# Performance work log

Hardware: AMD Instinct MI355X
Metric: run time of the kernel (lower is better)

Reference implementation:

```python
import jax, jax.numpy as jnp
import numpy as np

B, L, IN, D, H = 128, 64, 2, 256, 512  # batch, max_len, input_size, dense_size, hidden_size
A_S2S, A_PTR = H, D  # attention hidden sizes (defaults: hidden_size / dense_size)


def setup_inputs() -> dict:
    key = jax.random.key(0)
    ks = jax.random.split(key, 24)
    s = 0.05
    inp = {
        'inputs': jax.random.normal(ks[0], (B, L, IN), jnp.float32),
        'lengths': jax.random.randint(ks[1], (B,), L // 2, L + 1),
        'targets': jax.random.randint(ks[2], (B, L), 0, L),
        # input_dense: input_size -> dense_size
        'W_in': jax.random.normal(ks[3], (D, IN)) * s,
        'b_in': jnp.zeros((D,)),
        # encoder GRU (input D, hidden H), PyTorch layout [3H, in]
        'enc_Wi': jax.random.normal(ks[4], (3 * H, D)) * s,
        'enc_Wh': jax.random.normal(ks[5], (3 * H, H)) * s,
        'enc_bi': jnp.zeros((3 * H,)),
        'enc_bh': jnp.zeros((3 * H,)),
        # decoder GRU (input D+H, hidden H)
        'dec_Wi': jax.random.normal(ks[6], (3 * H, D + H)) * s,
        'dec_Wh': jax.random.normal(ks[7], (3 * H, H)) * s,
        'dec_bi': jnp.zeros((3 * H,)),
        'dec_bh': jnp.zeros((3 * H,)),
        # Bahdanau seq2seq attention: query_hidden = rnn_layers*H
        's2s_Wq': jax.random.normal(ks[8], (H, A_S2S)) * s,
        's2s_Wk': jax.random.normal(ks[9], (H, A_S2S)) * s,
        's2s_v': jax.random.normal(ks[10], (A_S2S,)) * s,
        # output_dense: hidden -> dense
        'W_out': jax.random.normal(ks[11], (D, H)) * s,
        'b_out': jnp.zeros((D,)),
        # Bahdanau pointer attention over dense_inputs
        'ptr_Wq': jax.random.normal(ks[12], (D, A_PTR)) * s,
        'ptr_Wk': jax.random.normal(ks[13], (D, A_PTR)) * s,
        'ptr_v': jax.random.normal(ks[14], (A_PTR,)) * s,
    }
    return inp


def _gru_cell(x, h, Wi, Wh, bi, bh):
    gi = x @ Wi.T + bi
    gh = h @ Wh.T + bh
    i_r, i_z, i_n = jnp.split(gi, 3, axis=-1)
    h_r, h_z, h_n = jnp.split(gh, 3, axis=-1)
    r = jax.nn.sigmoid(i_r + h_r)
    z = jax.nn.sigmoid(i_z + h_z)
    n = jnp.tanh(i_n + r * h_n)
    return (1.0 - z) * n + z * h


NEG = -1e9


def reference(inputs, lengths, targets, W_in, b_in, enc_Wi, enc_Wh, enc_bi, enc_bh,
              dec_Wi, dec_Wh, dec_bi, dec_bh, s2s_Wq, s2s_Wk, s2s_v,
              W_out, b_out, ptr_Wq, ptr_Wk, ptr_v):
    # teacher_forcing_prob fixed at 1.0 for determinism (uses targets each step)
    dense_inputs = inputs @ W_in.T + b_in            # [B, L, D]
    padding_mask = jnp.arange(L)[None, :] < lengths[:, None]  # [B, L] bool

    # ---- encoder (dynamic_rnn): run GRU over time, take hidden at lengths-1 ----
    def enc_step(h, x_t):
        h2 = _gru_cell(x_t, h, enc_Wi, enc_Wh, enc_bi, enc_bh)
        return h2, h2
    _, hs = jax.lax.scan(enc_step, jnp.zeros((B, H), dense_inputs.dtype),
                         dense_inputs.transpose(1, 0, 2))  # hs: [L, B, H]
    enc_out = hs.transpose(1, 0, 2) * padding_mask[:, :, None]  # zero padded steps
    hidden0 = hs[lengths - 1, jnp.arange(B)]  # final valid hidden, [B, H]

    # Precompute attention key projections (loop-invariant)
    enc_keys = enc_out @ s2s_Wk        # [B, L, A_S2S]
    ptr_keys = dense_inputs @ ptr_Wk   # [B, L, A_PTR]

    def dec_step(carry, inp):
        h, idx, step_mask = carry              # h [B,H], idx [B] int, step_mask [B,L]
        pm_i, tgt_i = inp                      # [B] bool, [B] int
        dec_in = dense_inputs[jnp.arange(B), idx]  # [B, D] gather
        m = pm_i[:, None] & padding_mask           # [B, L]
        # Bahdanau seq2seq attention, query = current hidden state
        q = h @ s2s_Wq                              # [B, A]
        scores = jnp.tanh(q[:, None, :] + enc_keys) @ s2s_v   # [B, L]
        scores = jnp.where(m, scores, NEG)
        w = jax.nn.softmax(scores, axis=-1)
        context = jnp.einsum('bl,blh->bh', w, enc_out)         # [B, H]
        x = jnp.concatenate([context, dec_in], axis=-1)        # [B, H+D]
        h_new = _gru_cell(x, h, dec_Wi, dec_Wh, dec_bi, dec_bh)
        # pointer attention over dense_inputs
        dense_out = h_new @ W_out.T + b_out                    # [B, D]
        p_mask = (step_mask > 0) & m
        pq = dense_out @ ptr_Wq
        plogit = jnp.tanh(pq[:, None, :] + ptr_keys) @ ptr_v   # [B, L]
        plogit = jnp.where(p_mask, plogit, NEG)
        pred = jnp.argmax(plogit, axis=-1)
        next_idx = tgt_i  # teacher forcing
        step_mask_new = step_mask * (1 - jax.nn.one_hot(next_idx, L, dtype=step_mask.dtype))
        return (h_new, next_idx, step_mask_new), (plogit, pred)

    carry0 = (hidden0, jnp.zeros((B,), jnp.int32),
              jnp.ones((B, L), jnp.int32))
    xs = (padding_mask.T, targets.T.astype(jnp.int32))
    _, (logits_t, preds_t) = jax.lax.scan(dec_step, carry0, xs)
    logits = logits_t.transpose(1, 0, 2)       # [B, L, L]
    predictions = preds_t.T                    # [B, L]
    return logits, predictions
```

## Files before the change

### kernel.cpp

```cpp
#include <hip/hip_runtime.h>

#define BB 128
#define LL 64
#define DD 256
#define HH 512
#define NEGC (-1e9f)

#define OFF_DENSE   0
#define OFF_ENCOUT  2097152
#define OFF_ENCKEYS 6291456
#define OFF_PTRKEYS 10485760
#define OFF_X       12582912
#define OFF_HB0     12681216
#define OFF_HB1     12746752
#define OFF_H0      12812288
#define OFF_Q       12877824
#define OFF_PQ      12943360
#define OFF_WQT     12976128
#define OFF_MT      13238272
#define OFF_BQ      13369344
#define OFF_SMASK   13369600

__device__ __forceinline__ float fast_tanh(float x) {
  float e = __expf(2.0f * x);
  return 1.0f - 2.0f / (e + 1.0f);
}
__device__ __forceinline__ float sigmoidf_(float x) {
  return 1.0f / (1.0f + __expf(-x));
}
__device__ __forceinline__ float wsum(float v) {
#pragma unroll
  for (int o = 32; o > 0; o >>= 1) v += __shfl_xor(v, o);
  return v;
}

#define D4(acc) fmaf(xv.x, w.x, fmaf(xv.y, w.y, fmaf(xv.z, w.z, fmaf(xv.w, w.w, acc))))


__global__ __launch_bounds__(256)
void k_init(const float* __restrict__ inp, const float* __restrict__ W_in,
            const float* __restrict__ b_in, float* __restrict__ dense,
            float* __restrict__ hb0, int* __restrict__ smask) {
  int idx = blockIdx.x * 256 + threadIdx.x;
  if (idx < BB * LL * DD) {
    int bl = idx >> 8, d = idx & 255;
    dense[idx] = fmaf(inp[bl * 2], W_in[d * 2], fmaf(inp[bl * 2 + 1], W_in[d * 2 + 1], b_in[d]));
  } else if (idx < BB * LL * DD + BB * HH) {
    hb0[idx - BB * LL * DD] = 0.f;
  } else if (idx < BB * LL * DD + BB * HH + BB * LL) {
    smask[idx - BB * LL * DD - BB * HH] = 1;
  }
}

__global__ __launch_bounds__(256)
void k_tr(const float* __restrict__ Wq, float* __restrict__ Wqt) {
  int idx = blockIdx.x * 256 + threadIdx.x;
  int h = idx >> 9, a = idx & 511;
  Wqt[a * 512 + h] = Wq[idx];
}

__global__ __launch_bounds__(512)
void k_mt(const float* __restrict__ W_out, const float* __restrict__ ptr_Wq,
          const float* __restrict__ b_out, float* __restrict__ Mt, float* __restrict__ bqv) {
  int a = blockIdx.x, tid = threadIdx.x;
  if (a < 256) {
    float acc = 0.f;
    for (int d = 0; d < 256; ++d) acc = fmaf(W_out[d * 512 + tid], ptr_Wq[d * 256 + a], acc);
    Mt[a * 512 + tid] = acc;
  } else if (tid < 256) {
    float acc = 0.f;
    for (int d = 0; d < 256; ++d) acc = fmaf(b_out[d], ptr_Wq[d * 256 + tid], acc);
    bqv[tid] = acc;
  }
}

__global__ __launch_bounds__(256)
void k_ptrkeys(const float* __restrict__ dense, const float* __restrict__ Wk,
               float* __restrict__ keys) {
  __shared__ float s[16 * 256];
  int r0 = blockIdx.x * 16, tid = threadIdx.x;
  for (int idx = tid; idx < 16 * 256; idx += 256) s[idx] = dense[r0 * 256 + idx];
  __syncthreads();
  float acc[16];
#pragma unroll
  for (int ri = 0; ri < 16; ++ri) acc[ri] = 0.f;
  for (int d = 0; d < 256; ++d) {
    float w = Wk[d * 256 + tid];
#pragma unroll
    for (int ri = 0; ri < 16; ++ri) acc[ri] = fmaf(s[ri * 256 + d], w, acc[ri]);
  }
#pragma unroll
  for (int ri = 0; ri < 16; ++ri) keys[(r0 + ri) * 256 + tid] = acc[ri];
}

__global__ __launch_bounds__(512)
void k_enckeys(const float* __restrict__ enc_out, const float* __restrict__ Wk,
               float* __restrict__ keys) {
  __shared__ float s[16 * 512];
  int r0 = blockIdx.x * 16, tid = threadIdx.x;
  for (int idx = tid; idx < 16 * 512; idx += 512) s[idx] = enc_out[r0 * 512 + idx];
  __syncthreads();
  float acc[16];
#pragma unroll
  for (int ri = 0; ri < 16; ++ri) acc[ri] = 0.f;
  for (int h = 0; h < 512; ++h) {
    float w = Wk[h * 512 + tid];
#pragma unroll
    for (int ri = 0; ri < 16; ++ri) acc[ri] = fmaf(s[ri * 512 + h], w, acc[ri]);
  }
#pragma unroll
  for (int ri = 0; ri < 16; ++ri) keys[(r0 + ri) * 512 + tid] = acc[ri];
}

__global__ __launch_bounds__(256)
void k_copy(const float* __restrict__ src, float* __restrict__ dst) {
  int idx = blockIdx.x * 256 + threadIdx.x;
  if (idx < BB * HH) dst[idx] = src[idx];
}

__global__ __launch_bounds__(256)
void k_enc(const float* __restrict__ dense, const float* __restrict__ hin,
           float* __restrict__ hout, const float* __restrict__ Wi,
           const float* __restrict__ Wh, const float* __restrict__ bi,
           const float* __restrict__ bh, const int* __restrict__ lengths,
           float* __restrict__ enc_out, float* __restrict__ h0, int t) {
  __shared__ float xs[16 * 772];
  __shared__ float part[2 * 16 * 8 * 8];
  const int tid = threadIdx.x;
  const int b0 = blockIdx.x * 16, u0 = blockIdx.y * 16;
  for (int idx = tid; idx < 16 * 768; idx += 256) {
    int bl = idx / 768, k = idx - bl * 768;
    xs[bl * 772 + k] = (k < 512) ? hin[(b0 + bl) * 512 + k]
                                 : dense[((b0 + bl) * 64 + t) * 256 + (k - 512)];
  }
  __syncthreads();
  {
    const int b_l = tid & 15, og = (tid >> 4) & 7, kp = tid >> 7;
    const int ua = u0 + og * 2;
    float ar0 = 0, az0 = 0, ain0 = 0, ahn0 = 0, ar1 = 0, az1 = 0, ain1 = 0, ahn1 = 0;
    const float* xr = xs + b_l * 772;
    const int k0 = kp * 384, k1 = k0 + 384;
    const int kA = (k1 < 512) ? k1 : 512;
    for (int k = k0; k < kA; k += 4) {
      float4 xv = *(const float4*)(xr + k);
      float4 w;
      w = *(const float4*)(Wh + (ua) * 512 + k);        ar0  = D4(ar0);
      w = *(const float4*)(Wh + (512 + ua) * 512 + k);  az0  = D4(az0);
      w = *(const float4*)(Wh + (1024 + ua) * 512 + k); ahn0 = D4(ahn0);
      w = *(const float4*)(Wh + (ua + 1) * 512 + k);    ar1  = D4(ar1);
      w = *(const float4*)(Wh + (513 + ua) * 512 + k);  az1  = D4(az1);
      w = *(const float4*)(Wh + (1025 + ua) * 512 + k); ahn1 = D4(ahn1);
    }
    const int kB = (k0 > 512) ? k0 : 512;
    for (int k = kB; k < k1; k += 4) {
      float4 xv = *(const float4*)(xr + k);
      float4 w;
      w = *(const float4*)(Wi + (ua) * 256 + k - 512);        ar0  = D4(ar0);
      w = *(const float4*)(Wi + (512 + ua) * 256 + k - 512);  az0  = D4(az0);
      w = *(const float4*)(Wi + (1024 + ua) * 256 + k - 512); ain0 = D4(ain0);
      w = *(const float4*)(Wi + (ua + 1) * 256 + k - 512);    ar1  = D4(ar1);
      w = *(const float4*)(Wi + (513 + ua) * 256 + k - 512);  az1  = D4(az1);
      w = *(const float4*)(Wi + (1025 + ua) * 256 + k - 512); ain1 = D4(ain1);
    }
    float* pp = part + ((kp * 16 + b_l) * 8 + og) * 8;
    pp[0] = ar0; pp[1] = az0; pp[2] = ain0; pp[3] = ahn0;
    pp[4] = ar1; pp[5] = az1; pp[6] = ain1; pp[7] = ahn1;
  }
  __syncthreads();
  {
    const int b_l = tid & 15, u_l = tid >> 4;
    const int og = u_l >> 1, uu = u_l & 1;
    const float* p0 = part + ((0 * 16 + b_l) * 8 + og) * 8 + uu * 4;
    const float* p1 = part + ((1 * 16 + b_l) * 8 + og) * 8 + uu * 4;
    float ar = p0[0] + p1[0], az = p0[1] + p1[1];
    float ain = p0[2] + p1[2], ahn = p0[3] + p1[3];
    const int u = u0 + u_l, b = b0 + b_l;
    float r = sigmoidf_(ar + bi[u] + bh[u]);
    float z = sigmoidf_(az + bi[512 + u] + bh[512 + u]);
    float n = fast_tanh(ain + bi[1024 + u] + r * (ahn + bh[1024 + u]));
    float hp = xs[b_l * 772 + u];
    float hn = (1.f - z) * n + z * hp;
    hout[b * 512 + u] = hn;
    int lenb = lengths[b];
    enc_out[(b * 64 + t) * 512 + u] = (t < lenb) ? hn : 0.f;
    if (t == lenb - 1) h0[b * 512 + u] = hn;
  }
}

__global__ __launch_bounds__(256)
void k_p1(int step, const float* __restrict__ qbuf, const float* __restrict__ pqbuf,
          const float* __restrict__ enc_keys, const float* __restrict__ ptr_keys,
          const float* __restrict__ enc_out, const float* __restrict__ dense,
          const float* __restrict__ s2s_v, const float* __restrict__ ptr_v,
          const int* __restrict__ lengths, const int* __restrict__ targets,
          int* __restrict__ smask, float* __restrict__ xbuf,
          float* __restrict__ logits, float* __restrict__ preds) {
  __shared__ float sq[512], sv[512], sl[64], wl[64];
  const int b = blockIdx.x, tid = threadIdx.x;
  const int wv = tid >> 6, ln = tid & 63;
  const int lenb = lengths[b];
  if (step > 0) {
    const int j = step - 1;
    sq[tid] = pqbuf[b * 256 + (tid & 255)];
    sv[tid] = ptr_v[tid & 255];
    __syncthreads();
#pragma unroll 4
    for (int li = 0; li < 16; ++li) {
      int l = wv * 16 + li;
      float acc = 0.f;
#pragma unroll
      for (int c = 0; c < 4; ++c) {
        int a = c * 64 + ln;
        acc = fmaf(fast_tanh(sq[a] + ptr_keys[(b * 64 + l) * 256 + a]), sv[a], acc);
      }
      acc = wsum(acc);
      if (ln == 0) sl[l] = acc;
    }
    __syncthreads();
    if (tid < 64) {
      int l = tid;
      bool pm = (j < lenb) && (l < lenb) && (smask[b * 64 + l] != 0);
      float v = pm ? sl[l] : NEGC;
      logits[(b * 64 + j) * 64 + l] = v;
      float bv = v; int bidx = l;
#pragma unroll
      for (int off = 32; off > 0; off >>= 1) {
        float ov = __shfl_xor(bv, off);
        int oi = __shfl_xor(bidx, off);
        if (ov > bv || (ov == bv && oi < bidx)) { bv = ov; bidx = oi; }
      }
      if (l == 0) preds[b * 64 + j] = (float)bidx;
    }
    __syncthreads();
    if (tid == 0) smask[b * 64 + targets[b * 64 + j]] = 0;
    __syncthreads();
  }
  if (step < 64) {
    const int i = step;
    sq[tid] = qbuf[b * 512 + tid];
    sq[tid + 256] = qbuf[b * 512 + 256 + tid];
    sv[tid] = s2s_v[tid];
    sv[tid + 256] = s2s_v[256 + tid];
    __syncthreads();
#pragma unroll 2
    for (int li = 0; li < 16; ++li) {
      int l = wv * 16 + li;
      float acc = 0.f;
#pragma unroll
      for (int c = 0; c < 8; ++c) {
        int a = c * 64 + ln;
        acc = fmaf(fast_tanh(sq[a] + enc_keys[(b * 64 + l) * 512 + a]), sv[a], acc);
      }
      acc = wsum(acc);
      if (ln == 0) sl[l] = ((i < lenb) && (l < lenb)) ? acc : NEGC;
    }
    __syncthreads();
    if (tid < 64) {
      float v = sl[tid];
      float m = v;
#pragma unroll
      for (int off = 32; off > 0; off >>= 1) m = fmaxf(m, __shfl_xor(m, off));
      float e = __expf(v - m);
      float s = e;
#pragma unroll
      for (int off = 32; off > 0; off >>= 1) s += __shfl_xor(s, off);
      wl[tid] = e / s;
    }
    __syncthreads();
    for (int hh = tid; hh < 512; hh += 256) {
      float c = 0.f;
#pragma unroll 8
      for (int l = 0; l < 64; ++l) c = fmaf(wl[l], enc_out[(b * 64 + l) * 512 + hh], c);
      xbuf[b * 768 + hh] = c;
    }
    int idx = (i == 0) ? 0 : targets[b * 64 + i - 1];
    xbuf[b * 768 + 512 + tid] = dense[(b * 64 + idx) * 256 + tid];
  }
}

__global__ __launch_bounds__(256)
void k_p2(const float* __restrict__ xbuf, const float* __restrict__ hin,
          float* __restrict__ hout, const float* __restrict__ Wi,
          const float* __restrict__ Wh, const float* __restrict__ bi,
          const float* __restrict__ bh) {
  __shared__ float xs[8 * 1284];
  __shared__ float part[4 * 8 * 8 * 8];
  const int tid = threadIdx.x;
  const int b0 = blockIdx.x * 8, u0 = blockIdx.y * 16;
  for (int idx = tid; idx < 8 * 1280; idx += 256) {
    int bl = idx / 1280, k = idx - bl * 1280;
    xs[bl * 1284 + k] = (k < 768) ? xbuf[(b0 + bl) * 768 + k]
                                  : hin[(b0 + bl) * 512 + (k - 768)];
  }
  __syncthreads();
  {
    const int b_l = tid & 7, og = (tid >> 3) & 7, kp = tid >> 6;
    const int ua = u0 + og * 2;
    float ar0 = 0, az0 = 0, ain0 = 0, ahn0 = 0, ar1 = 0, az1 = 0, ain1 = 0, ahn1 = 0;
    const float* xr = xs + b_l * 1284;
    const int k0 = kp * 320, k1 = k0 + 320;
    const int kA = (k1 < 768) ? k1 : 768;
    for (int k = k0; k < kA; k += 4) {
      float4 xv = *(const float4*)(xr + k);
      float4 w;
      w = *(const float4*)(Wi + (ua) * 768 + k);        ar0  = D4(ar0);
      w = *(const float4*)(Wi + (512 + ua) * 768 + k);  az0  = D4(az0);
      w = *(const float4*)(Wi + (1024 + ua) * 768 + k); ain0 = D4(ain0);
      w = *(const float4*)(Wi + (ua + 1) * 768 + k);    ar1  = D4(ar1);
      w = *(const float4*)(Wi + (513 + ua) * 768 + k);  az1  = D4(az1);
      w = *(const float4*)(Wi + (1025 + ua) * 768 + k); ain1 = D4(ain1);
    }
    const int kB = (k0 > 768) ? k0 : 768;
    for (int k = kB; k < k1; k += 4) {
      float4 xv = *(const float4*)(xr + k);
      float4 w;
      w = *(const float4*)(Wh + (ua) * 512 + k - 768);        ar0  = D4(ar0);
      w = *(const float4*)(Wh + (512 + ua) * 512 + k - 768);  az0  = D4(az0);
      w = *(const float4*)(Wh + (1024 + ua) * 512 + k - 768); ahn0 = D4(ahn0);
      w = *(const float4*)(Wh + (ua + 1) * 512 + k - 768);    ar1  = D4(ar1);
      w = *(const float4*)(Wh + (513 + ua) * 512 + k - 768);  az1  = D4(az1);
      w = *(const float4*)(Wh + (1025 + ua) * 512 + k - 768); ahn1 = D4(ahn1);
    }
    float* pp = part + ((kp * 8 + b_l) * 8 + og) * 8;
    pp[0] = ar0; pp[1] = az0; pp[2] = ain0; pp[3] = ahn0;
    pp[4] = ar1; pp[5] = az1; pp[6] = ain1; pp[7] = ahn1;
  }
  __syncthreads();
  if (tid < 128) {
    const int b_l = tid & 7, u_l = tid >> 3;
    const int og = u_l >> 1, uu = u_l & 1;
    float ar = 0, az = 0, ain = 0, ahn = 0;
#pragma unroll
    for (int kp = 0; kp < 4; ++kp) {
      const float* p = part + ((kp * 8 + b_l) * 8 + og) * 8 + uu * 4;
      ar += p[0]; az += p[1]; ain += p[2]; ahn += p[3];
    }
    const int u = u0 + u_l, b = b0 + b_l;
    float r = sigmoidf_(ar + bi[u] + bh[u]);
    float z = sigmoidf_(az + bi[512 + u] + bh[512 + u]);
    float n = fast_tanh(ain + bi[1024 + u] + r * (ahn + bh[1024 + u]));
    float hp = xs[b_l * 1284 + 768 + u];
    hout[b * 512 + u] = (1.f - z) * n + z * hp;
  }
}

__global__ __launch_bounds__(256)
void k_p3(const float* __restrict__ hsrc, const float* __restrict__ Wqt,
          const float* __restrict__ Mt, const float* __restrict__ bqv,
          float* __restrict__ qbuf, float* __restrict__ pqbuf) {
  __shared__ float hs[16 * 516];
  __shared__ float part[8 * 16 * 8];
  const int tid = threadIdx.x;
  const int b0 = blockIdx.x * 16, o0 = blockIdx.y * 8;
  for (int idx = tid; idx < 16 * 512; idx += 256) {
    int bl = idx >> 9, k = idx & 511;
    hs[bl * 516 + k] = hsrc[(b0 + bl) * 512 + k];
  }
  __syncthreads();
  {
    const int b_l = tid & 15, og = (tid >> 4) & 1, kp = tid >> 5;
    const int ob = o0 + og * 4;
    const float* w0 = (ob < 512) ? (Wqt + (ob) * 512) : (Mt + (ob - 512) * 512);
    const float* w1 = (ob < 512) ? (Wqt + (ob + 1) * 512) : (Mt + (ob - 511) * 512);
    const float* w2 = (ob < 512) ? (Wqt + (ob + 2) * 512) : (Mt + (ob - 510) * 512);
    const float* w3 = (ob < 512) ? (Wqt + (ob + 3) * 512) : (Mt + (ob - 509) * 512);
    float a0 = 0, a1 = 0, a2 = 0, a3 = 0;
    const float* xr = hs + b_l * 516;
    const int k0 = kp * 64;
    for (int k = k0; k < k0 + 64; k += 4) {
      float4 xv = *(const float4*)(xr + k);
      float4 w;
      w = *(const float4*)(w0 + k); a0 = D4(a0);
      w = *(const float4*)(w1 + k); a1 = D4(a1);
      w = *(const float4*)(w2 + k); a2 = D4(a2);
      w = *(const float4*)(w3 + k); a3 = D4(a3);
    }
    float* pp = part + ((kp * 16 + b_l) * 8 + og * 4);
    pp[0] = a0; pp[1] = a1; pp[2] = a2; pp[3] = a3;
  }
  __syncthreads();
  if (tid < 128) {
    const int b_l = tid & 15, o_l = tid >> 4;
    float s = 0.f;
#pragma unroll
    for (int kp = 0; kp < 8; ++kp) s += part[(kp * 16 + b_l) * 8 + o_l];
    const int b = b0 + b_l, o = o0 + o_l;
    if (o < 512) qbuf[b * 512 + o] = s;
    else pqbuf[b * 256 + (o - 512)] = s + bqv[o - 512];
  }
}

extern "C" void kernel_launch(void* const* d_in, const int* in_sizes, int n_in,
                              void* d_out, int out_size, void* d_ws, size_t ws_size,
                              hipStream_t stream) {
  (void)in_sizes; (void)n_in; (void)out_size; (void)ws_size;
  const float* inputs  = (const float*)d_in[0];
  const int*   lengths = (const int*)d_in[1];
  const int*   targets = (const int*)d_in[2];
  const float* W_in    = (const float*)d_in[3];
  const float* b_in    = (const float*)d_in[4];
  const float* enc_Wi  = (const float*)d_in[5];
  const float* enc_Wh  = (const float*)d_in[6];
  const float* enc_bi  = (const float*)d_in[7];
  const float* enc_bh  = (const float*)d_in[8];
  const float* dec_Wi  = (const float*)d_in[9];
  const float* dec_Wh  = (const float*)d_in[10];
  const float* dec_bi  = (const float*)d_in[11];
  const float* dec_bh  = (const float*)d_in[12];
  const float* s2s_Wq  = (const float*)d_in[13];
  const float* s2s_Wk  = (const float*)d_in[14];
  const float* s2s_v   = (const float*)d_in[15];
  const float* W_out   = (const float*)d_in[16];
  const float* b_out   = (const float*)d_in[17];
  const float* ptr_Wq  = (const float*)d_in[18];
  const float* ptr_Wk  = (const float*)d_in[19];
  const float* ptr_v   = (const float*)d_in[20];

  float* ws = (float*)d_ws;
  float* dense    = ws + OFF_DENSE;
  float* enc_out  = ws + OFF_ENCOUT;
  float* enc_keys = ws + OFF_ENCKEYS;
  float* ptr_keys = ws + OFF_PTRKEYS;
  float* xbuf     = ws + OFF_X;
  float* hb0      = ws + OFF_HB0;
  float* hb1      = ws + OFF_HB1;
  float* h0       = ws + OFF_H0;
  float* qbuf     = ws + OFF_Q;
  float* pqbuf    = ws + OFF_PQ;
  float* Wqt      = ws + OFF_WQT;
  float* Mt       = ws + OFF_MT;
  float* bqv      = ws + OFF_BQ;
  int*   smask    = (int*)(ws + OFF_SMASK);

  float* logits = (float*)d_out;
  float* preds  = (float*)d_out + BB * LL * LL;

  k_init<<<8480, 256, 0, stream>>>(inputs, W_in, b_in, dense, hb0, smask);
  k_tr<<<1024, 256, 0, stream>>>(s2s_Wq, Wqt);
  k_mt<<<257, 512, 0, stream>>>(W_out, ptr_Wq, b_out, Mt, bqv);
  k_ptrkeys<<<512, 256, 0, stream>>>(dense, ptr_Wk, ptr_keys);

  for (int t = 0; t < 64; ++t) {
    float* hi = (t & 1) ? hb1 : hb0;
    float* ho = (t & 1) ? hb0 : hb1;
    k_enc<<<dim3(8, 32), 256, 0, stream>>>(dense, hi, ho, enc_Wi, enc_Wh, enc_bi,
                                           enc_bh, lengths, enc_out, h0, t);
  }
  k_copy<<<256, 256, 0, stream>>>(h0, hb0);
  k_enckeys<<<512, 512, 0, stream>>>(enc_out, s2s_Wk, enc_keys);
  k_p3<<<dim3(8, 96), 256, 0, stream>>>(hb0, Wqt, Mt, bqv, qbuf, pqbuf);

  for (int i = 0; i < 64; ++i) {
    float* hi = (i & 1) ? hb1 : hb0;
    float* ho = (i & 1) ? hb0 : hb1;
    k_p1<<<128, 256, 0, stream>>>(i, qbuf, pqbuf, enc_keys, ptr_keys, enc_out, dense,
                                  s2s_v, ptr_v, lengths, targets, smask, xbuf,
                                  logits, preds);
    k_p2<<<dim3(16, 32), 256, 0, stream>>>(xbuf, hi, ho, dec_Wi, dec_Wh, dec_bi, dec_bh);
    k_p3<<<dim3(8, 96), 256, 0, stream>>>(ho, Wqt, Mt, bqv, qbuf, pqbuf);
  }
  k_p1<<<128, 256, 0, stream>>>(64, qbuf, pqbuf, enc_keys, ptr_keys, enc_out, dense,
                                s2s_v, ptr_v, lengths, targets, smask, xbuf,
                                logits, preds);
}
```

Baseline: 7.077 ms.

## Fuse all phases into one persistent cooperative kernel with grid barriers

Replaces roughly 260 separate kernel launches (encoder steps, key projections, decoder attention/GRU/query phases) with a single cooperative persistent kernel of 256 blocks. A software grid barrier built on atomics separates the phases. The step mask becomes a per-block 64-bit register bitmask instead of a global int array. The goal is to remove per-launch overhead and gaps between the sequential recurrent steps. In exchange it relies on all blocks being co-resident and a spin barrier whose per-barrier cost may be comparable to a launch, and it changes the work split per phase.

```diff
diff --git a/kernel.cpp b/kernel.cpp
--- a/kernel.cpp
+++ b/kernel.cpp
@@ -5,6 +5,9 @@
 #define DD 256
 #define HH 512
 #define NEGC (-1e9f)
+
+#define NBLK 256
+#define NTHR 512
 
 #define OFF_DENSE   0
 #define OFF_ENCOUT  2097152
@@ -19,7 +22,7 @@
 #define OFF_WQT     12976128
 #define OFF_MT      13238272
 #define OFF_BQ      13369344
-#define OFF_SMASK   13369600
+#define OFF_BAR     13369600
 
 __device__ __forceinline__ float fast_tanh(float x) {
   float e = __expf(2.0f * x);
@@ -36,387 +39,49 @@
 
 #define D4(acc) fmaf(xv.x, w.x, fmaf(xv.y, w.y, fmaf(xv.z, w.z, fmaf(xv.w, w.w, acc))))
 
-
-__global__ __launch_bounds__(256)
-void k_init(const float* __restrict__ inp, const float* __restrict__ W_in,
-            const float* __restrict__ b_in, float* __restrict__ dense,
-            float* __restrict__ hb0, int* __restrict__ smask) {
-  int idx = blockIdx.x * 256 + threadIdx.x;
-  if (idx < BB * LL * DD) {
-    int bl = idx >> 8, d = idx & 255;
-    dense[idx] = fmaf(inp[bl * 2], W_in[d * 2], fmaf(inp[bl * 2 + 1], W_in[d * 2 + 1], b_in[d]));
-  } else if (idx < BB * LL * DD + BB * HH) {
-    hb0[idx - BB * LL * DD] = 0.f;
-  } else if (idx < BB * LL * DD + BB * HH + BB * LL) {
-    smask[idx - BB * LL * DD - BB * HH] = 1;
-  }
-}
-
-__global__ __launch_bounds__(256)
-void k_tr(const float* __restrict__ Wq, float* __restrict__ Wqt) {
-  int idx = blockIdx.x * 256 + threadIdx.x;
-  int h = idx >> 9, a = idx & 511;
-  Wqt[a * 512 + h] = Wq[idx];
-}
-
-__global__ __launch_bounds__(512)
-void k_mt(const float* __restrict__ W_out, const float* __restrict__ ptr_Wq,
-          const float* __restrict__ b_out, float* __restrict__ Mt, float* __restrict__ bqv) {
-  int a = blockIdx.x, tid = threadIdx.x;
-  if (a < 256) {
-    float acc = 0.f;
-    for (int d = 0; d < 256; ++d) acc = fmaf(W_out[d * 512 + tid], ptr_Wq[d * 256 + a], acc);
-    Mt[a * 512 + tid] = acc;
-  } else if (tid < 256) {
-    float acc = 0.f;
-    for (int d = 0; d < 256; ++d) acc = fmaf(b_out[d], ptr_Wq[d * 256 + tid], acc);
-    bqv[tid] = acc;
-  }
-}
-
-__global__ __launch_bounds__(256)
-void k_ptrkeys(const float* __restrict__ dense, const float* __restrict__ Wk,
-               float* __restrict__ keys) {
-  __shared__ float s[16 * 256];
-  int r0 = blockIdx.x * 16, tid = threadIdx.x;
-  for (int idx = tid; idx < 16 * 256; idx += 256) s[idx] = dense[r0 * 256 + idx];
+struct MegaArgs {
+  const float* inputs; const int* lengths; const int* targets;
+  const float* W_in; const float* b_in;
+  const float* enc_Wi; const float* enc_Wh; const float* enc_bi; const float* enc_bh;
+  const float* dec_Wi; const float* dec_Wh; const float* dec_bi; const float* dec_bh;
+  const float* s2s_Wq; const float* s2s_Wk; const float* s2s_v;
+  const float* W_out; const float* b_out;
+  const float* ptr_Wq; const float* ptr_Wk; const float* ptr_v;
+  float* ws; float* logits; float* preds;
+};
+
+__device__ __forceinline__ void gridbar(unsigned* cnt, unsigned* gen) {
   __syncthreads();
-  float acc[16];
-#pragma unroll
-  for (int ri = 0; ri < 16; ++ri) acc[ri] = 0.f;
-  for (int d = 0; d < 256; ++d) {
-    float w = Wk[d * 256 + tid];
-#pragma unroll
-    for (int ri = 0; ri < 16; ++ri) acc[ri] = fmaf(s[ri * 256 + d], w, acc[ri]);
-  }
-#pragma unroll
-  for (int ri = 0; ri < 16; ++ri) keys[(r0 + ri) * 256 + tid] = acc[ri];
-}
-
-__global__ __launch_bounds__(512)
-void k_enckeys(const float* __restrict__ enc_out, const float* __restrict__ Wk,
-               float* __restrict__ keys) {
-  __shared__ float s[16 * 512];
-  int r0 = blockIdx.x * 16, tid = threadIdx.x;
-  for (int idx = tid; idx < 16 * 512; idx += 512) s[idx] = enc_out[r0 * 512 + idx];
+  if (threadIdx.x == 0) {
+    unsigned g = __hip_atomic_load(gen, __ATOMIC_RELAXED, __HIP_MEMORY_SCOPE_AGENT);
+    unsigned v = __hip_atomic_fetch_add(cnt, 1u, __ATOMIC_ACQ_REL, __HIP_MEMORY_SCOPE_AGENT);
+    if (v == (unsigned)(NBLK - 1)) {
+      __hip_atomic_store(cnt, 0u, __ATOMIC_RELAXED, __HIP_MEMORY_SCOPE_AGENT);
+      __hip_atomic_store(gen, g + 1u, __ATOMIC_RELEASE, __HIP_MEMORY_SCOPE_AGENT);
+    } else {
+      while (__hip_atomic_load(gen, __ATOMIC_RELAXED, __HIP_MEMORY_SCOPE_AGENT) == g)
+        __builtin_amdgcn_s_sleep(2);
+      (void)__hip_atomic_load(gen, __ATOMIC_ACQUIRE, __HIP_MEMORY_SCOPE_AGENT);
+    }
+  }
   __syncthreads();
-  float acc[16];
-#pragma unroll
-  for (int ri = 0; ri < 16; ++ri) acc[ri] = 0.f;
-  for (int h = 0; h < 512; ++h) {
-    float w = Wk[h * 512 + tid];
-#pragma unroll
-    for (int ri = 0; ri < 16; ++ri) acc[ri] = fmaf(s[ri * 512 + h], w, acc[ri]);
-  }
-#pragma unroll
-  for (int ri = 0; ri < 16; ++ri) keys[(r0 + ri) * 512 + tid] = acc[ri];
-}
-
-__global__ __launch_bounds__(256)
-void k_copy(const float* __restrict__ src, float* __restrict__ dst) {
-  int idx = blockIdx.x * 256 + threadIdx.x;
-  if (idx < BB * HH) dst[idx] = src[idx];
-}
-
-__global__ __launch_bounds__(256)
-void k_enc(const float* __restrict__ dense, const float* __restrict__ hin,
-           float* __restrict__ hout, const float* __restrict__ Wi,
-           const float* __restrict__ Wh, const float* __restrict__ bi,
-           const float* __restrict__ bh, const int* __restrict__ lengths,
-           float* __restrict__ enc_out, float* __restrict__ h0, int t) {
-  __shared__ float xs[16 * 772];
-  __shared__ float part[2 * 16 * 8 * 8];
+}
+
+struct SMem {
+  union {
+    struct { float xs[16 * 772];  float part[4 * 16 * 8 * 8]; } e;
+    struct { float xs[16 * 1284]; float part[4 * 16 * 8 * 8]; } p2;
+    struct { float hs[16 * 516];  float part[4 * 16 * 24];    } p3;
+    struct { float s[32 * 256]; } pk;
+    struct { float s[16 * 512]; } ek;
+    struct { float sq[512]; float sv[512]; float sl[64]; float wl[64]; } a1;
+  };
+};
+
+__global__ __launch_bounds__(NTHR) void mega(MegaArgs a) {
+  const int blk = blockIdx.x;
   const int tid = threadIdx.x;
-  const int b0 = blockIdx.x * 16, u0 = blockIdx.y * 16;
-  for (int idx = tid; idx < 16 * 768; idx += 256) {
-    int bl = idx / 768, k = idx - bl * 768;
-    xs[bl * 772 + k] = (k < 512) ? hin[(b0 + bl) * 512 + k]
-                                 : dense[((b0 + bl) * 64 + t) * 256 + (k - 512)];
-  }
-  __syncthreads();
-  {
-    const int b_l = tid & 15, og = (tid >> 4) & 7, kp = tid >> 7;
-    const int ua = u0 + og * 2;
-    float ar0 = 0, az0 = 0, ain0 = 0, ahn0 = 0, ar1 = 0, az1 = 0, ain1 = 0, ahn1 = 0;
-    const float* xr = xs + b_l * 772;
-    const int k0 = kp * 384, k1 = k0 + 384;
-    const int kA = (k1 < 512) ? k1 : 512;
-    for (int k = k0; k < kA; k += 4) {
-      float4 xv = *(const float4*)(xr + k);
-      float4 w;
-      w = *(const float4*)(Wh + (ua) * 512 + k);        ar0  = D4(ar0);
-      w = *(const float4*)(Wh + (512 + ua) * 512 + k);  az0  = D4(az0);
-      w = *(const float4*)(Wh + (1024 + ua) * 512 + k); ahn0 = D4(ahn0);
-      w = *(const float4*)(Wh + (ua + 1) * 512 + k);    ar1  = D4(ar1);
-      w = *(const float4*)(Wh + (513 + ua) * 512 + k);  az1  = D4(az1);
-      w = *(const float4*)(Wh + (1025 + ua) * 512 + k); ahn1 = D4(ahn1);
-    }
-    const int kB = (k0 > 512) ? k0 : 512;
-    for (int k = kB; k < k1; k += 4) {
-      float4 xv = *(const float4*)(xr + k);
-      float4 w;
-      w = *(const float4*)(Wi + (ua) * 256 + k - 512);        ar0  = D4(ar0);
-      w = *(const float4*)(Wi + (512 + ua) * 256 + k - 512);  az0  = D4(az0);
-      w = *(const float4*)(Wi + (1024 + ua) * 256 + k - 512); ain0 = D4(ain0);
-      w = *(const float4*)(Wi + (ua + 1) * 256 + k - 512);    ar1  = D4(ar1);
-      w = *(const float4*)(Wi + (513 + ua) * 256 + k - 512);  az1  = D4(az1);
-      w = *(const float4*)(Wi + (1025 + ua) * 256 + k - 512); ain1 = D4(ain1);
-    }
-    float* pp = part + ((kp * 16 + b_l) * 8 + og) * 8;
-    pp[0] = ar0; pp[1] = az0; pp[2] = ain0; pp[3] = ahn0;
-    pp[4] = ar1; pp[5] = az1; pp[6] = ain1; pp[7] = ahn1;
-  }
-  __syncthreads();
-  {
-    const int b_l = tid & 15, u_l = tid >> 4;
-    const int og = u_l >> 1, uu = u_l & 1;
-    const float* p0 = part + ((0 * 16 + b_l) * 8 + og) * 8 + uu * 4;
-    const float* p1 = part + ((1 * 16 + b_l) * 8 + og) * 8 + uu * 4;
-    float ar = p0[0] + p1[0], az = p0[1] + p1[1];
-    float ain = p0[2] + p1[2], ahn = p0[3] + p1[3];
-    const int u = u0 + u_l, b = b0 + b_l;
-    float r = sigmoidf_(ar + bi[u] + bh[u]);
-    float z = sigmoidf_(az + bi[512 + u] + bh[512 + u]);
-    float n = fast_tanh(ain + bi[1024 + u] + r * (ahn + bh[1024 + u]));
-    float hp = xs[b_l * 772 + u];
-    float hn = (1.f - z) * n + z * hp;
-    hout[b * 512 + u] = hn;
-    int lenb = lengths[b];
-    enc_out[(b * 64 + t) * 512 + u] = (t < lenb) ? hn : 0.f;
-    if (t == lenb - 1) h0[b * 512 + u] = hn;
-  }
-}
-
-__global__ __launch_bounds__(256)
-void k_p1(int step, const float* __restrict__ qbuf, const float* __restrict__ pqbuf,
-          const float* __restrict__ enc_keys, const float* __restrict__ ptr_keys,
-          const float* __restrict__ enc_out, const float* __restrict__ dense,
-          const float* __restrict__ s2s_v, const float* __restrict__ ptr_v,
-          const int* __restrict__ lengths, const int* __restrict__ targets,
-          int* __restrict__ smask, float* __restrict__ xbuf,
-          float* __restrict__ logits, float* __restrict__ preds) {
-  __shared__ float sq[512], sv[512], sl[64], wl[64];
-  const int b = blockIdx.x, tid = threadIdx.x;
-  const int wv = tid >> 6, ln = tid & 63;
-  const int lenb = lengths[b];
-  if (step > 0) {
-    const int j = step - 1;
-    sq[tid] = pqbuf[b * 256 + (tid & 255)];
-    sv[tid] = ptr_v[tid & 255];
-    __syncthreads();
-#pragma unroll 4
-    for (int li = 0; li < 16; ++li) {
-      int l = wv * 16 + li;
-      float acc = 0.f;
-#pragma unroll
-      for (int c = 0; c < 4; ++c) {
-        int a = c * 64 + ln;
-        acc = fmaf(fast_tanh(sq[a] + ptr_keys[(b * 64 + l) * 256 + a]), sv[a], acc);
-      }
-      acc = wsum(acc);
-      if (ln == 0) sl[l] = acc;
-    }
-    __syncthreads();
-    if (tid < 64) {
-      int l = tid;
-      bool pm = (j < lenb) && (l < lenb) && (smask[b * 64 + l] != 0);
-      float v = pm ? sl[l] : NEGC;
-      logits[(b * 64 + j) * 64 + l] = v;
-      float bv = v; int bidx = l;
-#pragma unroll
-      for (int off = 32; off > 0; off >>= 1) {
-        float ov = __shfl_xor(bv, off);
-        int oi = __shfl_xor(bidx, off);
-        if (ov > bv || (ov == bv && oi < bidx)) { bv = ov; bidx = oi; }
-      }
-      if (l == 0) preds[b * 64 + j] = (float)bidx;
-    }
-    __syncthreads();
-    if (tid == 0) smask[b * 64 + targets[b * 64 + j]] = 0;
-    __syncthreads();
-  }
-  if (step < 64) {
-    const int i = step;
-    sq[tid] = qbuf[b * 512 + tid];
-    sq[tid + 256] = qbuf[b * 512 + 256 + tid];
-    sv[tid] = s2s_v[tid];
-    sv[tid + 256] = s2s_v[256 + tid];
-    __syncthreads();
-#pragma unroll 2
-    for (int li = 0; li < 16; ++li) {
-      int l = wv * 16 + li;
-      float acc = 0.f;
-#pragma unroll
-      for (int c = 0; c < 8; ++c) {
-        int a = c * 64 + ln;
-        acc = fmaf(fast_tanh(sq[a] + enc_keys[(b * 64 + l) * 512 + a]), sv[a], acc);
-      }
-      acc = wsum(acc);
-      if (ln == 0) sl[l] = ((i < lenb) && (l < lenb)) ? acc : NEGC;
-    }
-    __syncthreads();
-    if (tid < 64) {
-      float v = sl[tid];
-      float m = v;
-#pragma unroll
-      for (int off = 32; off > 0; off >>= 1) m = fmaxf(m, __shfl_xor(m, off));
-      float e = __expf(v - m);
-      float s = e;
-#pragma unroll
-      for (int off = 32; off > 0; off >>= 1) s += __shfl_xor(s, off);
-      wl[tid] = e / s;
-    }
-    __syncthreads();
-    for (int hh = tid; hh < 512; hh += 256) {
-      float c = 0.f;
-#pragma unroll 8
-      for (int l = 0; l < 64; ++l) c = fmaf(wl[l], enc_out[(b * 64 + l) * 512 + hh], c);
-      xbuf[b * 768 + hh] = c;
-    }
-    int idx = (i == 0) ? 0 : targets[b * 64 + i - 1];
-    xbuf[b * 768 + 512 + tid] = dense[(b * 64 + idx) * 256 + tid];
-  }
-}
-
-__global__ __launch_bounds__(256)
-void k_p2(const float* __restrict__ xbuf, const float* __restrict__ hin,
-          float* __restrict__ hout, const float* __restrict__ Wi,
-          const float* __restrict__ Wh, const float* __restrict__ bi,
-          const float* __restrict__ bh) {
-  __shared__ float xs[8 * 1284];
-  __shared__ float part[4 * 8 * 8 * 8];
-  const int tid = threadIdx.x;
-  const int b0 = blockIdx.x * 8, u0 = blockIdx.y * 16;
-  for (int idx = tid; idx < 8 * 1280; idx += 256) {
-    int bl = idx / 1280, k = idx - bl * 1280;
-    xs[bl * 1284 + k] = (k < 768) ? xbuf[(b0 + bl) * 768 + k]
-                                  : hin[(b0 + bl) * 512 + (k - 768)];
-  }
-  __syncthreads();
-  {
-    const int b_l = tid & 7, og = (tid >> 3) & 7, kp = tid >> 6;
-    const int ua = u0 + og * 2;
-    float ar0 = 0, az0 = 0, ain0 = 0, ahn0 = 0, ar1 = 0, az1 = 0, ain1 = 0, ahn1 = 0;
-    const float* xr = xs + b_l * 1284;
-    const int k0 = kp * 320, k1 = k0 + 320;
-    const int kA = (k1 < 768) ? k1 : 768;
-    for (int k = k0; k < kA; k += 4) {
-      float4 xv = *(const float4*)(xr + k);
-      float4 w;
-      w = *(const float4*)(Wi + (ua) * 768 + k);        ar0  = D4(ar0);
-      w = *(const float4*)(Wi + (512 + ua) * 768 + k);  az0  = D4(az0);
-      w = *(const float4*)(Wi + (1024 + ua) * 768 + k); ain0 = D4(ain0);
-      w = *(const float4*)(Wi + (ua + 1) * 768 + k);    ar1  = D4(ar1);
-      w = *(const float4*)(Wi + (513 + ua) * 768 + k);  az1  = D4(az1);
-      w = *(const float4*)(Wi + (1025 + ua) * 768 + k); ain1 = D4(ain1);
-    }
-    const int kB = (k0 > 768) ? k0 : 768;
-    for (int k = kB; k < k1; k += 4) {
-      float4 xv = *(const float4*)(xr + k);
-      float4 w;
-      w = *(const float4*)(Wh + (ua) * 512 + k - 768);        ar0  = D4(ar0);
-      w = *(const float4*)(Wh + (512 + ua) * 512 + k - 768);  az0  = D4(az0);
-      w = *(const float4*)(Wh + (1024 + ua) * 512 + k - 768); ahn0 = D4(ahn0);
-      w = *(const float4*)(Wh + (ua + 1) * 512 + k - 768);    ar1  = D4(ar1);
-      w = *(const float4*)(Wh + (513 + ua) * 512 + k - 768);  az1  = D4(az1);
-      w = *(const float4*)(Wh + (1025 + ua) * 512 + k - 768); ahn1 = D4(ahn1);
-    }
-    float* pp = part + ((kp * 8 + b_l) * 8 + og) * 8;
-    pp[0] = ar0; pp[1] = az0; pp[2] = ain0; pp[3] = ahn0;
-    pp[4] = ar1; pp[5] = az1; pp[6] = ain1; pp[7] = ahn1;
-  }
-  __syncthreads();
-  if (tid < 128) {
-    const int b_l = tid & 7, u_l = tid >> 3;
-    const int og = u_l >> 1, uu = u_l & 1;
-    float ar = 0, az = 0, ain = 0, ahn = 0;
-#pragma unroll
-    for (int kp = 0; kp < 4; ++kp) {
-      const float* p = part + ((kp * 8 + b_l) * 8 + og) * 8 + uu * 4;
-      ar += p[0]; az += p[1]; ain += p[2]; ahn += p[3];
-    }
-    const int u = u0 + u_l, b = b0 + b_l;
-    float r = sigmoidf_(ar + bi[u] + bh[u]);
-    float z = sigmoidf_(az + bi[512 + u] + bh[512 + u]);
-    float n = fast_tanh(ain + bi[1024 + u] + r * (ahn + bh[1024 + u]));
-    float hp = xs[b_l * 1284 + 768 + u];
-    hout[b * 512 + u] = (1.f - z) * n + z * hp;
-  }
-}
-
-__global__ __launch_bounds__(256)
-void k_p3(const float* __restrict__ hsrc, const float* __restrict__ Wqt,
-          const float* __restrict__ Mt, const float* __restrict__ bqv,
-          float* __restrict__ qbuf, float* __restrict__ pqbuf) {
-  __shared__ float hs[16 * 516];
-  __shared__ float part[8 * 16 * 8];
-  const int tid = threadIdx.x;
-  const int b0 = blockIdx.x * 16, o0 = blockIdx.y * 8;
-  for (int idx = tid; idx < 16 * 512; idx += 256) {
-    int bl = idx >> 9, k = idx & 511;
-    hs[bl * 516 + k] = hsrc[(b0 + bl) * 512 + k];
-  }
-  __syncthreads();
-  {
-    const int b_l = tid & 15, og = (tid >> 4) & 1, kp = tid >> 5;
-    const int ob = o0 + og * 4;
-    const float* w0 = (ob < 512) ? (Wqt + (ob) * 512) : (Mt + (ob - 512) * 512);
-    const float* w1 = (ob < 512) ? (Wqt + (ob + 1) * 512) : (Mt + (ob - 511) * 512);
-    const float* w2 = (ob < 512) ? (Wqt + (ob + 2) * 512) : (Mt + (ob - 510) * 512);
-    const float* w3 = (ob < 512) ? (Wqt + (ob + 3) * 512) : (Mt + (ob - 509) * 512);
-    float a0 = 0, a1 = 0, a2 = 0, a3 = 0;
-    const float* xr = hs + b_l * 516;
-    const int k0 = kp * 64;
-    for (int k = k0; k < k0 + 64; k += 4) {
-      float4 xv = *(const float4*)(xr + k);
-      float4 w;
-      w = *(const float4*)(w0 + k); a0 = D4(a0);
-      w = *(const float4*)(w1 + k); a1 = D4(a1);
-      w = *(const float4*)(w2 + k); a2 = D4(a2);
-      w = *(const float4*)(w3 + k); a3 = D4(a3);
-    }
-    float* pp = part + ((kp * 16 + b_l) * 8 + og * 4);
-    pp[0] = a0; pp[1] = a1; pp[2] = a2; pp[3] = a3;
-  }
-  __syncthreads();
-  if (tid < 128) {
-    const int b_l = tid & 15, o_l = tid >> 4;
-    float s = 0.f;
-#pragma unroll
-    for (int kp = 0; kp < 8; ++kp) s += part[(kp * 16 + b_l) * 8 + o_l];
-    const int b = b0 + b_l, o = o0 + o_l;
-    if (o < 512) qbuf[b * 512 + o] = s;
-    else pqbuf[b * 256 + (o - 512)] = s + bqv[o - 512];
-  }
-}
-
-extern "C" void kernel_launch(void* const* d_in, const int* in_sizes, int n_in,
-                              void* d_out, int out_size, void* d_ws, size_t ws_size,
-                              hipStream_t stream) {
-  (void)in_sizes; (void)n_in; (void)out_size; (void)ws_size;
-  const float* inputs  = (const float*)d_in[0];
-  const int*   lengths = (const int*)d_in[1];
-  const int*   targets = (const int*)d_in[2];
-  const float* W_in    = (const float*)d_in[3];
-  const float* b_in    = (const float*)d_in[4];
-  const float* enc_Wi  = (const float*)d_in[5];
-  const float* enc_Wh  = (const float*)d_in[6];
-  const float* enc_bi  = (const float*)d_in[7];
-  const float* enc_bh  = (const float*)d_in[8];
-  const float* dec_Wi  = (const float*)d_in[9];
-  const float* dec_Wh  = (const float*)d_in[10];
-  const float* dec_bi  = (const float*)d_in[11];
-  const float* dec_bh  = (const float*)d_in[12];
-  const float* s2s_Wq  = (const float*)d_in[13];
-  const float* s2s_Wk  = (const float*)d_in[14];
-  const float* s2s_v   = (const float*)d_in[15];
-  const float* W_out   = (const float*)d_in[16];
-  const float* b_out   = (const float*)d_in[17];
-  const float* ptr_Wq  = (const float*)d_in[18];
-  const float* ptr_Wk  = (const float*)d_in[19];
-  const float* ptr_v   = (const float*)d_in[20];
-
-  float* ws = (float*)d_ws;
+  float* ws = a.ws;
   float* dense    = ws + OFF_DENSE;
   float* enc_out  = ws + OFF_ENCOUT;
   float* enc_keys = ws + OFF_ENCKEYS;
@@ -430,36 +95,367 @@
   float* Wqt      = ws + OFF_WQT;
   float* Mt       = ws + OFF_MT;
   float* bqv      = ws + OFF_BQ;
-  int*   smask    = (int*)(ws + OFF_SMASK);
-
-  float* logits = (float*)d_out;
-  float* preds  = (float*)d_out + BB * LL * LL;
-
-  k_init<<<8480, 256, 0, stream>>>(inputs, W_in, b_in, dense, hb0, smask);
-  k_tr<<<1024, 256, 0, stream>>>(s2s_Wq, Wqt);
-  k_mt<<<257, 512, 0, stream>>>(W_out, ptr_Wq, b_out, Mt, bqv);
-  k_ptrkeys<<<512, 256, 0, stream>>>(dense, ptr_Wk, ptr_keys);
-
+  unsigned* cnt   = (unsigned*)(ws + OFF_BAR);
+  unsigned* gen   = (unsigned*)(ws + OFF_BAR) + 64;
+
+  __shared__ SMem sm;
+
+  unsigned long long alive = ~0ull;
+
+  for (int idx = blk * NTHR + tid; idx < BB * LL * DD; idx += NBLK * NTHR) {
+    int bl = idx >> 8, d = idx & 255;
+    dense[idx] = fmaf(a.inputs[bl * 2], a.W_in[d * 2],
+                 fmaf(a.inputs[bl * 2 + 1], a.W_in[d * 2 + 1], a.b_in[d]));
+  }
+  for (int idx = blk * NTHR + tid; idx < 512 * 512; idx += NBLK * NTHR) {
+    int h = idx >> 9, q = idx & 511;
+    Wqt[q * 512 + h] = a.s2s_Wq[idx];
+  }
+  for (int idx = blk * NTHR + tid; idx < BB * HH; idx += NBLK * NTHR) hb0[idx] = 0.f;
+  {
+    float acc = 0.f;
+    for (int d = 0; d < 256; ++d)
+      acc = fmaf(a.W_out[d * 512 + tid], a.ptr_Wq[d * 256 + blk], acc);
+    Mt[blk * 512 + tid] = acc;
+  }
+  if (blk == 0 && tid < 256) {
+    float acc = 0.f;
+    for (int d = 0; d < 256; ++d) acc = fmaf(a.b_out[d], a.ptr_Wq[d * 256 + tid], acc);
+    bqv[tid] = acc;
+  }
+  gridbar(cnt, gen);
+
+  {
+    const int r0 = blk * 32;
+    for (int idx = tid; idx < 32 * 256; idx += NTHR) sm.pk.s[idx] = dense[r0 * 256 + idx];
+    __syncthreads();
+    const int col = tid & 255, rg = tid >> 8;
+    float acc[16];
+#pragma unroll
+    for (int ri = 0; ri < 16; ++ri) acc[ri] = 0.f;
+    const float* srow = sm.pk.s + rg * 16 * 256;
+    for (int d = 0; d < 256; ++d) {
+      float w = a.ptr_Wk[d * 256 + col];
+#pragma unroll
+      for (int ri = 0; ri < 16; ++ri) acc[ri] = fmaf(srow[ri * 256 + d], w, acc[ri]);
+    }
+#pragma unroll
+    for (int ri = 0; ri < 16; ++ri)
+      ptr_keys[(r0 + rg * 16 + ri) * 256 + col] = acc[ri];
+  }
+  gridbar(cnt, gen);
+
+#pragma unroll 1
   for (int t = 0; t < 64; ++t) {
-    float* hi = (t & 1) ? hb1 : hb0;
-    float* ho = (t & 1) ? hb0 : hb1;
-    k_enc<<<dim3(8, 32), 256, 0, stream>>>(dense, hi, ho, enc_Wi, enc_Wh, enc_bi,
-                                           enc_bh, lengths, enc_out, h0, t);
-  }
-  k_copy<<<256, 256, 0, stream>>>(h0, hb0);
-  k_enckeys<<<512, 512, 0, stream>>>(enc_out, s2s_Wk, enc_keys);
-  k_p3<<<dim3(8, 96), 256, 0, stream>>>(hb0, Wqt, Mt, bqv, qbuf, pqbuf);
-
+    const int b0 = (blk >> 5) * 16, u0 = (blk & 31) * 16;
+    const float* hin = (t & 1) ? hb1 : hb0;
+    float* hout = (t & 1) ? hb0 : hb1;
+    for (int idx = tid; idx < 16 * 768; idx += NTHR) {
+      int bl = idx / 768, k = idx - bl * 768;
+      sm.e.xs[bl * 772 + k] = (k < 512) ? hin[(b0 + bl) * 512 + k]
+                                        : dense[((b0 + bl) * 64 + t) * 256 + (k - 512)];
+    }
+    __syncthreads();
+    {
+      const int b_l = tid & 15, og = (tid >> 4) & 7, kp = tid >> 7;
+      const int ua = u0 + og * 2;
+      float ar0 = 0, az0 = 0, ain0 = 0, ahn0 = 0, ar1 = 0, az1 = 0, ain1 = 0, ahn1 = 0;
+      const float* xr = sm.e.xs + b_l * 772;
+      const int k0 = kp * 192, k1 = k0 + 192;
+      const int kA = (k1 < 512) ? k1 : 512;
+      for (int k = k0; k < kA; k += 4) {
+        float4 xv = *(const float4*)(xr + k);
+        float4 w;
+        w = *(const float4*)(a.enc_Wh + (ua) * 512 + k);        ar0  = D4(ar0);
+        w = *(const float4*)(a.enc_Wh + (512 + ua) * 512 + k);  az0  = D4(az0);
+        w = *(const float4*)(a.enc_Wh + (1024 + ua) * 512 + k); ahn0 = D4(ahn0);
+        w = *(const float4*)(a.enc_Wh + (ua + 1) * 512 + k);    ar1  = D4(ar1);
+        w = *(const float4*)(a.enc_Wh + (513 + ua) * 512 + k);  az1  = D4(az1);
+        w = *(const float4*)(a.enc_Wh + (1025 + ua) * 512 + k); ahn1 = D4(ahn1);
+      }
+      const int kB = (k0 > 512) ? k0 : 512;
+      for (int k = kB; k < k1; k += 4) {
+        float4 xv = *(const float4*)(xr + k);
+        float4 w;
+        w = *(const float4*)(a.enc_Wi + (ua) * 256 + k - 512);        ar0  = D4(ar0);
+        w = *(const float4*)(a.enc_Wi + (512 + ua) * 256 + k - 512);  az0  = D4(az0);
+        w = *(const float4*)(a.enc_Wi + (1024 + ua) * 256 + k - 512); ain0 = D4(ain0);
+        w = *(const float4*)(a.enc_Wi + (ua + 1) * 256 + k - 512);    ar1  = D4(ar1);
+        w = *(const float4*)(a.enc_Wi + (513 + ua) * 256 + k - 512);  az1  = D4(az1);
+        w = *(const float4*)(a.enc_Wi + (1025 + ua) * 256 + k - 512); ain1 = D4(ain1);
+      }
+      float* pp = sm.e.part + ((kp * 16 + b_l) * 8 + og) * 8;
+      pp[0] = ar0; pp[1] = az0; pp[2] = ain0; pp[3] = ahn0;
+      pp[4] = ar1; pp[5] = az1; pp[6] = ain1; pp[7] = ahn1;
+    }
+    __syncthreads();
+    if (tid < 256) {
+      const int b_l = tid & 15, u_l = tid >> 4;
+      const int og = u_l >> 1, uu = u_l & 1;
+      float ar = 0, az = 0, ain = 0, ahn = 0;
+#pragma unroll
+      for (int kp = 0; kp < 4; ++kp) {
+        const float* p = sm.e.part + ((kp * 16 + b_l) * 8 + og) * 8 + uu * 4;
+        ar += p[0]; az += p[1]; ain += p[2]; ahn += p[3];
+      }
+      const int u = u0 + u_l, b = b0 + b_l;
+      float r = sigmoidf_(ar + a.enc_bi[u] + a.enc_bh[u]);
+      float z = sigmoidf_(az + a.enc_bi[512 + u] + a.enc_bh[512 + u]);
+      float n = fast_tanh(ain + a.enc_bi[1024 + u] + r * (ahn + a.enc_bh[1024 + u]));
+      float hp = sm.e.xs[b_l * 772 + u];
+      float hn = (1.f - z) * n + z * hp;
+      hout[b * 512 + u] = hn;
+      int lenb = a.lengths[b];
+      enc_out[(b * 64 + t) * 512 + u] = (t < lenb) ? hn : 0.f;
+      if (t == lenb - 1) h0[b * 512 + u] = hn;
+    }
+    gridbar(cnt, gen);
+  }
+
+  auto phaseA0 = [&](const float* hsrc) {
+    const int b0 = (blk >> 5) * 16, o0 = (blk & 31) * 24;
+    for (int idx = tid; idx < 16 * 512; idx += NTHR) {
+      int bl = idx >> 9, k = idx & 511;
+      sm.p3.hs[bl * 516 + k] = hsrc[(b0 + bl) * 512 + k];
+    }
+    __syncthreads();
+    {
+      const int b_l = tid & 15, og = (tid >> 4) & 7, kp = tid >> 7;
+      const int oa = o0 + og * 3;
+      const float* w0 = (oa     < 512) ? (Wqt + oa * 512)       : (Mt + (oa - 512) * 512);
+      const float* w1 = (oa + 1 < 512) ? (Wqt + (oa + 1) * 512) : (Mt + (oa - 511) * 512);
+      const float* w2 = (oa + 2 < 512) ? (Wqt + (oa + 2) * 512) : (Mt + (oa - 510) * 512);
+      float c0 = 0, c1 = 0, c2 = 0;
+      const float* xr = sm.p3.hs + b_l * 516;
+      const int k0 = kp * 128;
+      for (int k = k0; k < k0 + 128; k += 4) {
+        float4 xv = *(const float4*)(xr + k);
+        float4 w;
+        w = *(const float4*)(w0 + k); c0 = D4(c0);
+        w = *(const float4*)(w1 + k); c1 = D4(c1);
+        w = *(const float4*)(w2 + k); c2 = D4(c2);
+      }
+      float* pp = sm.p3.part + (kp * 16 + b_l) * 24 + og * 3;
+      pp[0] = c0; pp[1] = c1; pp[2] = c2;
+    }
+    __syncthreads();
+    if (tid < 384) {
+      const int b_l = tid & 15, o_l = tid >> 4;
+      float s = 0.f;
+#pragma unroll
+      for (int kp = 0; kp < 4; ++kp) s += sm.p3.part[(kp * 16 + b_l) * 24 + o_l];
+      const int b = b0 + b_l, o = o0 + o_l;
+      if (o < 512) qbuf[b * 512 + o] = s;
+      else pqbuf[b * 256 + (o - 512)] = s + bqv[o - 512];
+    }
+  };
+
+  auto phaseA1 = [&](int step) {
+    if (blk >= BB) return;
+    const int b = blk;
+    const int wv = tid >> 6, ln = tid & 63;
+    const int lenb = a.lengths[b];
+    if (step > 0) {
+      const int j = step - 1;
+      if (tid < 256) { sm.a1.sq[tid] = pqbuf[b * 256 + tid]; sm.a1.sv[tid] = a.ptr_v[tid]; }
+      __syncthreads();
+#pragma unroll
+      for (int li = 0; li < 8; ++li) {
+        int l = wv * 8 + li;
+        float acc = 0.f;
+#pragma unroll
+        for (int c = 0; c < 4; ++c) {
+          int q = c * 64 + ln;
+          acc = fmaf(fast_tanh(sm.a1.sq[q] + ptr_keys[(b * 64 + l) * 256 + q]), sm.a1.sv[q], acc);
+        }
+        acc = wsum(acc);
+        if (ln == 0) sm.a1.sl[l] = acc;
+      }
+      __syncthreads();
+      if (tid < 64) {
+        int l = tid;
+        bool pm = (j < lenb) && (l < lenb) && ((alive >> l) & 1ull);
+        float v = pm ? sm.a1.sl[l] : NEGC;
+        a.logits[(b * 64 + j) * 64 + l] = v;
+        float bv = v; int bidx = l;
+#pragma unroll
+        for (int off = 32; off > 0; off >>= 1) {
+          float ov = __shfl_xor(bv, off);
+          int oi = __shfl_xor(bidx, off);
+          if (ov > bv || (ov == bv && oi < bidx)) { bv = ov; bidx = oi; }
+        }
+        if (l == 0) a.preds[b * 64 + j] = (float)bidx;
+      }
+      alive &= ~(1ull << (unsigned)a.targets[b * 64 + j]);
+      __syncthreads();
+    }
+    if (step < 64) {
+      const int i = step;
+      sm.a1.sq[tid] = qbuf[b * 512 + tid];
+      sm.a1.sv[tid] = a.s2s_v[tid];
+      __syncthreads();
+#pragma unroll
+      for (int li = 0; li < 8; ++li) {
+        int l = wv * 8 + li;
+        float acc = 0.f;
+#pragma unroll
+        for (int c = 0; c < 8; ++c) {
+          int q = c * 64 + ln;
+          acc = fmaf(fast_tanh(sm.a1.sq[q] + enc_keys[(b * 64 + l) * 512 + q]), sm.a1.sv[q], acc);
+        }
+        acc = wsum(acc);
+        if (ln == 0) sm.a1.sl[l] = ((i < lenb) && (l < lenb)) ? acc : NEGC;
+      }
+      __syncthreads();
+      if (tid < 64) {
+        float v = sm.a1.sl[tid];
+        float m = v;
+#pragma unroll
+        for (int off = 32; off > 0; off >>= 1) m = fmaxf(m, __shfl_xor(m, off));
+        float e = __expf(v - m);
+        float s = e;
+#pragma unroll
+        for (int off = 32; off > 0; off >>= 1) s += __shfl_xor(s, off);
+        sm.a1.wl[tid] = e / s;
+      }
+      __syncthreads();
+      {
+        float c = 0.f;
+#pragma unroll 8
+        for (int l = 0; l < 64; ++l) c = fmaf(sm.a1.wl[l], enc_out[(b * 64 + l) * 512 + tid], c);
+        xbuf[b * 768 + tid] = c;
+      }
+      if (tid < 256) {
+        int di = (i == 0) ? 0 : a.targets[b * 64 + i - 1];
+        xbuf[b * 768 + 512 + tid] = dense[(b * 64 + di) * 256 + tid];
+      }
+    }
+  };
+
+#pragma unroll 1
+  for (int rep = 0; rep < 2; ++rep) {
+    const int r0 = (blk * 2 + rep) * 16;
+    for (int idx = tid; idx < 16 * 512; idx += NTHR) sm.ek.s[idx] = enc_out[r0 * 512 + idx];
+    __syncthreads();
+    float acc[16];
+#pragma unroll
+    for (int ri = 0; ri < 16; ++ri) acc[ri] = 0.f;
+    for (int h = 0; h < 512; ++h) {
+      float w = a.s2s_Wk[h * 512 + tid];
+#pragma unroll
+      for (int ri = 0; ri < 16; ++ri) acc[ri] = fmaf(sm.ek.s[ri * 512 + h], w, acc[ri]);
+    }
+#pragma unroll
+    for (int ri = 0; ri < 16; ++ri) enc_keys[(r0 + ri) * 512 + tid] = acc[ri];
+    __syncthreads();
+  }
+  phaseA0(h0);
+  gridbar(cnt, gen);
+
+#pragma unroll 1
   for (int i = 0; i < 64; ++i) {
-    float* hi = (i & 1) ? hb1 : hb0;
-    float* ho = (i & 1) ? hb0 : hb1;
-    k_p1<<<128, 256, 0, stream>>>(i, qbuf, pqbuf, enc_keys, ptr_keys, enc_out, dense,
-                                  s2s_v, ptr_v, lengths, targets, smask, xbuf,
-                                  logits, preds);
-    k_p2<<<dim3(16, 32), 256, 0, stream>>>(xbuf, hi, ho, dec_Wi, dec_Wh, dec_bi, dec_bh);
-    k_p3<<<dim3(8, 96), 256, 0, stream>>>(ho, Wqt, Mt, bqv, qbuf, pqbuf);
-  }
-  k_p1<<<128, 256, 0, stream>>>(64, qbuf, pqbuf, enc_keys, ptr_keys, enc_out, dense,
-                                s2s_v, ptr_v, lengths, targets, smask, xbuf,
-                                logits, preds);
-}
+    phaseA1(i);
+    gridbar(cnt, gen);
+    {
+      const int b0 = (blk >> 5) * 16, u0 = (blk & 31) * 16;
+      const float* hin = (i == 0) ? h0 : ((i & 1) ? hb1 : hb0);
+      float* hout = (i & 1) ? hb0 : hb1;
+      for (int idx = tid; idx < 16 * 1280; idx += NTHR) {
+        int bl = idx / 1280, k = idx - bl * 1280;
+        sm.p2.xs[bl * 1284 + k] = (k < 768) ? xbuf[(b0 + bl) * 768 + k]
+                                            : hin[(b0 + bl) * 512 + (k - 768)];
+      }
+      __syncthreads();
+      {
+        const int b_l = tid & 15, og = (tid >> 4) & 7, kp = tid >> 7;
+        const int ua = u0 + og * 2;
+        float ar0 = 0, az0 = 0, ain0 = 0, ahn0 = 0, ar1 = 0, az1 = 0, ain1 = 0, ahn1 = 0;
+        const float* xr = sm.p2.xs + b_l * 1284;
+        const int k0 = kp * 320, k1 = k0 + 320;
+        const int kA = (k1 < 768) ? k1 : 768;
+        for (int k = k0; k < kA; k += 4) {
+          float4 xv = *(const float4*)(xr + k);
+          float4 w;
+          w = *(const float4*)(a.dec_Wi + (ua) * 768 + k);        ar0  = D4(ar0);
+          w = *(const float4*)(a.dec_Wi + (512 + ua) * 768 + k);  az0  = D4(az0);
+          w = *(const float4*)(a.dec_Wi + (1024 + ua) * 768 + k); ain0 = D4(ain0);
+          w = *(const float4*)(a.dec_Wi + (ua + 1) * 768 + k);    ar1  = D4(ar1);
+          w = *(const float4*)(a.dec_Wi + (513 + ua) * 768 + k);  az1  = D4(az1);
+          w = *(const float4*)(a.dec_Wi + (1025 + ua) * 768 + k); ain1 = D4(ain1);
+        }
+        const int kB = (k0 > 768) ? k0 : 768;
+        for (int k = kB; k < k1; k += 4) {
+          float4 xv = *(const float4*)(xr + k);
+          float4 w;
+          w = *(const float4*)(a.dec_Wh + (ua) * 512 + k - 768);        ar0  = D4(ar0);
+          w = *(const float4*)(a.dec_Wh + (512 + ua) * 512 + k - 768);  az0  = D4(az0);
+          w = *(const float4*)(a.dec_Wh + (1024 + ua) * 512 + k - 768); ahn0 = D4(ahn0);
+          w = *(const float4*)(a.dec_Wh + (ua + 1) * 512 + k - 768);    ar1  = D4(ar1);
+          w = *(const float4*)(a.dec_Wh + (513 + ua) * 512 + k - 768);  az1  = D4(az1);
+          w = *(const float4*)(a.dec_Wh + (1025 + ua) * 512 + k - 768); ahn1 = D4(ahn1);
+        }
+        float* pp = sm.p2.part + ((kp * 16 + b_l) * 8 + og) * 8;
+        pp[0] = ar0; pp[1] = az0; pp[2] = ain0; pp[3] = ahn0;
+        pp[4] = ar1; pp[5] = az1; pp[6] = ain1; pp[7] = ahn1;
+      }
+      __syncthreads();
+      if (tid < 256) {
+        const int b_l = tid & 15, u_l = tid >> 4;
+        const int og = u_l >> 1, uu = u_l & 1;
+        float ar = 0, az = 0, ain = 0, ahn = 0;
+#pragma unroll
+        for (int kp = 0; kp < 4; ++kp) {
+          const float* p = sm.p2.part + ((kp * 16 + b_l) * 8 + og) * 8 + uu * 4;
+          ar += p[0]; az += p[1]; ain += p[2]; ahn += p[3];
+        }
+        const int u = u0 + u_l, b = b0 + b_l;
+        float r = sigmoidf_(ar + a.dec_bi[u] + a.dec_bh[u]);
+        float z = sigmoidf_(az + a.dec_bi[512 + u] + a.dec_bh[512 + u]);
+        float n = fast_tanh(ain + a.dec_bi[1024 + u] + r * (ahn + a.dec_bh[1024 + u]));
+        float hp = sm.p2.xs[b_l * 1284 + 768 + u];
+        hout[b * 512 + u] = (1.f - z) * n + z * hp;
+      }
+    }
+    gridbar(cnt, gen);
+    phaseA0((i & 1) ? hb0 : hb1);
+    gridbar(cnt, gen);
+  }
+  phaseA1(64);
+}
+
+extern "C" void kernel_launch(void* const* d_in, const int* in_sizes, int n_in,
+                              void* d_out, int out_size, void* d_ws, size_t ws_size,
+                              hipStream_t stream) {
+  (void)in_sizes; (void)n_in; (void)out_size; (void)ws_size;
+  MegaArgs ma;
+  ma.inputs  = (const float*)d_in[0];
+  ma.lengths = (const int*)d_in[1];
+  ma.targets = (const int*)d_in[2];
+  ma.W_in    = (const float*)d_in[3];
+  ma.b_in    = (const float*)d_in[4];
+  ma.enc_Wi  = (const float*)d_in[5];
+  ma.enc_Wh  = (const float*)d_in[6];
+  ma.enc_bi  = (const float*)d_in[7];
+  ma.enc_bh  = (const float*)d_in[8];
+  ma.dec_Wi  = (const float*)d_in[9];
+  ma.dec_Wh  = (const float*)d_in[10];
+  ma.dec_bi  = (const float*)d_in[11];
+  ma.dec_bh  = (const float*)d_in[12];
+  ma.s2s_Wq  = (const float*)d_in[13];
+  ma.s2s_Wk  = (const float*)d_in[14];
+  ma.s2s_v   = (const float*)d_in[15];
+  ma.W_out   = (const float*)d_in[16];
+  ma.b_out   = (const float*)d_in[17];
+  ma.ptr_Wq  = (const float*)d_in[18];
+  ma.ptr_Wk  = (const float*)d_in[19];
+  ma.ptr_v   = (const float*)d_in[20];
+  ma.ws     = (float*)d_ws;
+  ma.logits = (float*)d_out;
+  ma.preds  = (float*)d_out + BB * LL * LL;
+
+  hipMemsetAsync((float*)d_ws + OFF_BAR, 0, 512, stream);
+
+  void* kp[] = { &ma };
+  hipLaunchCooperativeKernel(reinterpret_cast<const void*>(&mega),
+                             dim3(NBLK), dim3(NTHR), kp, 0, stream);
+}
```

New measurement: 11.13 ms. 1.57x slower.
